# Optimization experiments

Measured on AMD Instinct MI355X. Metric: run time of the kernel, lower is better.

## Reference

```python
import jax, jax.numpy as jnp
import numpy as np

N = 50000      # num nodes
E0 = 400000    # raw directed edges
F = 64         # latent_dim (in and per-head out)
H = 2          # num_heads
L = 2          # num_layers
NEG_SLOPE = 0.2


def _build_edges(src_raw, dst_raw):
    # dgl.to_bidirected(dgl.graph((src,dst))) then add_self_loop
    s = np.asarray(src_raw, dtype=np.int64)
    d = np.asarray(dst_raw, dtype=np.int64)
    s2 = np.concatenate([s, d])
    d2 = np.concatenate([d, s])
    code = np.unique(s2 * N + d2)                      # dedupe (bidirected simple graph)
    s2, d2 = code // N, code % N
    keep = s2 != d2                                    # drop existing self loops
    s2, d2 = s2[keep], d2[keep]
    loops = np.arange(N, dtype=np.int64)
    s2 = np.concatenate([s2, loops])
    d2 = np.concatenate([d2, loops])
    return jnp.asarray(s2, jnp.int32), jnp.asarray(d2, jnp.int32)


def setup_inputs() -> dict:
    key = jax.random.key(0)
    kh, ks, kd, kw1, kb1, kw2, kb2, ka = jax.random.split(key, 8)
    src_raw = jax.random.randint(ks, (E0,), 0, N, dtype=jnp.int32)
    dst_raw = jax.random.randint(kd, (E0,), 0, N, dtype=jnp.int32)
    src, dst = _build_edges(np.asarray(src_raw), np.asarray(dst_raw))
    h = jax.random.normal(kh, (N, F), dtype=jnp.float32)
    scale = 1.0 / np.sqrt(F)
    Wsrc = jax.random.normal(kw1, (L, F, H * F), dtype=jnp.float32) * scale
    bsrc = jnp.zeros((L, H * F), dtype=jnp.float32)
    Wdst = jax.random.normal(kw2, (L, F, H * F), dtype=jnp.float32) * scale
    bdst = jnp.zeros((L, H * F), dtype=jnp.float32)
    attn = jax.random.normal(ka, (L, H, F), dtype=jnp.float32) * scale
    return {"h": h, "Wsrc": Wsrc, "bsrc": bsrc, "Wdst": Wdst, "bdst": bdst,
            "attn": attn, "src": src, "dst": dst}


def _gatv2_layer(h, Wsrc, bsrc, Wdst, bdst, attn, src, dst):
    # h: [N,F] -> per-head projections [N,H,F]
    fs = (h @ Wsrc + bsrc).reshape(N, H, F)
    fd = (h @ Wdst + bdst).reshape(N, H, F)
    # per-edge GATv2 logits: a^T leaky_relu(W_s h_u + W_d h_v)
    e = jax.nn.leaky_relu(fs[src] + fd[dst], NEG_SLOPE)      # [E,H,F]
    logits = jnp.einsum("ehf,hf->eh", e, attn)               # [E,H]
    # edge-softmax over incoming edges of each dst node
    m = jax.ops.segment_max(logits, dst, num_segments=N)     # [N,H]
    ex = jnp.exp(logits - m[dst])
    denom = jax.ops.segment_sum(ex, dst, num_segments=N)     # [N,H]
    alpha = ex / denom[dst]                                  # [E,H]
    # scatter-weighted aggregation
    out = jax.ops.segment_sum(alpha[:, :, None] * fs[src], dst, num_segments=N)  # [N,H,F]
    return out.mean(axis=1)                                  # head mean -> [N,F]


def reference(h, Wsrc, bsrc, Wdst, bdst, attn, src, dst):
    for l in range(L):
        h = _gatv2_layer(h, Wsrc[l], bsrc[l], Wdst[l], bdst[l], attn[l], src, dst)
    return h
```

## Files before the change

### kernel.cpp

```cpp
#include <hip/hip_runtime.h>


#define RLN2 1.4426950408889634f

typedef _Float16 half8v __attribute__((ext_vector_type(8)));
typedef _Float16 half2v __attribute__((ext_vector_type(2)));

template <int CTRL>
__device__ __forceinline__ float dpp_add(float x) {
  return x + __int_as_float(__builtin_amdgcn_update_dpp(
                 0, __float_as_int(x), CTRL, 0xF, 0xF, true));
}

__device__ __forceinline__ float xor16_add(float x) {
  return x + __int_as_float(
                 __builtin_amdgcn_ds_swizzle(__float_as_int(x), 0x401F));
}

__device__ __forceinline__ float dot2(half2v a, half2v b, float c) {
#if __has_builtin(__builtin_amdgcn_fdot2)
  return __builtin_amdgcn_fdot2(a, b, c, false);
#else
  return fmaf((float)a.x, (float)b.x, fmaf((float)a.y, (float)b.y, c));
#endif
}

__global__ void rowstart_kernel(const int* __restrict__ src,
                                int* __restrict__ row_start, int EM, int n) {
  int v = blockIdx.x * blockDim.x + threadIdx.x;
  if (v > n) return;
  if (v == n) { row_start[n] = EM; return; }
  int lo = 0, hi = EM;
  while (lo < hi) {
    int mid = (lo + hi) >> 1;
    if (src[mid] < v) lo = mid + 1; else hi = mid;
  }
  row_start[v] = lo;
}

__global__ __launch_bounds__(512) void proj2_kernel(
    const float* __restrict__ hin, const float* __restrict__ Ws,
    const float* __restrict__ bs, const float* __restrict__ Wd,
    const float* __restrict__ bd, _Float16* __restrict__ fs16,
    _Float16* __restrict__ fd16, int n) {
  __shared__ float lds[12544];
  int tid = threadIdx.x;
  int tile = blockIdx.x >> 1;
  int half = blockIdx.x & 1;
  int fb = half * 32;
  int row0 = tile * 64;

  const float4* Ws4 = (const float4*)Ws;
  const float4* Wd4 = (const float4*)Wd;
#pragma unroll
  for (int t = 0; t < 2; ++t) {
    int g = tid + t * 512;
    int k = g >> 4, part = (g >> 3) & 1, c4 = g & 7;
    int srcf4 = k * 32 + part * 16 + half * 8 + c4;
    float4 vs = Ws4[srcf4];
    float4 vd = Wd4[srcf4];
    int base = k * 64 + 8 * c4 + part;
    lds[base + 0] = vs.x; lds[base + 2] = vs.y;
    lds[base + 4] = vs.z; lds[base + 6] = vs.w;
    lds[4096 + base + 0] = vd.x; lds[4096 + base + 2] = vd.y;
    lds[4096 + base + 4] = vd.z; lds[4096 + base + 6] = vd.w;
  }
  const float4* h4 = (const float4*)hin;
#pragma unroll
  for (int t = 0; t < 2; ++t) {
    int idx = tid + t * 512;
    int r = idx >> 4, c = idx & 15;
    int rr = min(row0 + r, n - 1);
    *(float4*)&lds[8192 + r * 68 + c * 4] = h4[(size_t)rr * 16 + c];
  }
  __syncthreads();

  const float* WsL = lds;
  const float* WdL = lds + 4096;
  const float* hL = lds + 8192;

  int jh = tid & 15;
  int rg = tid >> 4;
  int r0 = rg * 2;

  float4 as0 = make_float4(0, 0, 0, 0), as1 = make_float4(0, 0, 0, 0);
  float4 ad0 = make_float4(0, 0, 0, 0), ad1 = make_float4(0, 0, 0, 0);

#pragma unroll 4
  for (int k4 = 0; k4 < 16; ++k4) {
    float4 hv0 = *(const float4*)&hL[r0 * 68 + k4 * 4];
    float4 hv1 = *(const float4*)&hL[(r0 + 1) * 68 + k4 * 4];
    float h0a[4] = {hv0.x, hv0.y, hv0.z, hv0.w};
    float h1a[4] = {hv1.x, hv1.y, hv1.z, hv1.w};
#pragma unroll
    for (int kk = 0; kk < 4; ++kk) {
      int k = k4 * 4 + kk;
      float4 ws = *(const float4*)&WsL[k * 64 + jh * 4];
      float4 wd = *(const float4*)&WdL[k * 64 + jh * 4];
      as0.x = fmaf(h0a[kk], ws.x, as0.x); as0.y = fmaf(h0a[kk], ws.y, as0.y);
      as0.z = fmaf(h0a[kk], ws.z, as0.z); as0.w = fmaf(h0a[kk], ws.w, as0.w);
      as1.x = fmaf(h1a[kk], ws.x, as1.x); as1.y = fmaf(h1a[kk], ws.y, as1.y);
      as1.z = fmaf(h1a[kk], ws.z, as1.z); as1.w = fmaf(h1a[kk], ws.w, as1.w);
      ad0.x = fmaf(h0a[kk], wd.x, ad0.x); ad0.y = fmaf(h0a[kk], wd.y, ad0.y);
      ad0.z = fmaf(h0a[kk], wd.z, ad0.z); ad0.w = fmaf(h0a[kk], wd.w, ad0.w);
      ad1.x = fmaf(h1a[kk], wd.x, ad1.x); ad1.y = fmaf(h1a[kk], wd.y, ad1.y);
      ad1.z = fmaf(h1a[kk], wd.z, ad1.z); ad1.w = fmaf(h1a[kk], wd.w, ad1.w);
    }
  }

  int j0 = fb + 2 * jh, j1 = j0 + 1;
  float4 bsv = make_float4(bs[j0], bs[64 + j0], bs[j1], bs[64 + j1]);
  float4 bdv = make_float4(bd[j0], bd[64 + j0], bd[j1], bd[64 + j1]);
  int c0 = j0 >> 2, o = j0 & 3;
  int base = c0 * 8 + o;
#pragma unroll
  for (int r = 0; r < 2; ++r) {
    int rr = row0 + r0 + r;
    if (rr < n) {
      float4 a = r ? as1 : as0;
      float4 d = r ? ad1 : ad0;
      half2v s_h0 = {(_Float16)(a.x + bsv.x), (_Float16)(a.z + bsv.z)};
      half2v s_h1 = {(_Float16)(a.y + bsv.y), (_Float16)(a.w + bsv.w)};
      half2v d_h0 = {(_Float16)(d.x + bdv.x), (_Float16)(d.z + bdv.z)};
      half2v d_h1 = {(_Float16)(d.y + bdv.y), (_Float16)(d.w + bdv.w)};
      *(half2v*)&fs16[(size_t)rr * 128 + base] = s_h0;
      *(half2v*)&fs16[(size_t)rr * 128 + base + 4] = s_h1;
      *(half2v*)&fd16[(size_t)rr * 128 + base] = d_h0;
      *(half2v*)&fd16[(size_t)rr * 128 + base + 4] = d_h1;
    }
  }
}

__global__ __launch_bounds__(256) void gat_node_kernel(
    const _Float16* __restrict__ fs16, const _Float16* __restrict__ fd16,
    const float* __restrict__ attn, const int* __restrict__ row_start,
    const int* __restrict__ nbr, float* __restrict__ out, int n) {
  int wid = (int)((blockIdx.x * 256 + threadIdx.x) >> 6);
  int lane = threadIdx.x & 63;
  if (wid >= n) return;
  int lp = lane & 15;
  int slot = lane >> 4;

  half2v a0lo = {(_Float16)(attn[4 * lp] * RLN2),
                 (_Float16)(attn[4 * lp + 1] * RLN2)};
  half2v a0hi = {(_Float16)(attn[4 * lp + 2] * RLN2),
                 (_Float16)(attn[4 * lp + 3] * RLN2)};
  half2v a1lo = {(_Float16)(attn[64 + 4 * lp] * RLN2),
                 (_Float16)(attn[64 + 4 * lp + 1] * RLN2)};
  half2v a1hi = {(_Float16)(attn[64 + 4 * lp + 2] * RLN2),
                 (_Float16)(attn[64 + 4 * lp + 3] * RLN2)};
  const half8v c02 = {(_Float16)0.2f, (_Float16)0.2f, (_Float16)0.2f,
                      (_Float16)0.2f, (_Float16)0.2f, (_Float16)0.2f,
                      (_Float16)0.2f, (_Float16)0.2f};

  const half8v* fsC = (const half8v*)fs16;
  const half8v* fdC = (const half8v*)fd16;
  half8v fdh = fdC[(size_t)wid * 16 + lp];

  float4 acc0 = make_float4(0, 0, 0, 0), acc1 = make_float4(0, 0, 0, 0);
  float d0 = 0.f, d1 = 0.f;

#define EDGE_COMPUTE(xv, kill_cond)                                        \
  {                                                                        \
    half8v t = (xv) + fdh;                                                 \
    half8v m = __builtin_elementwise_max(t, t * c02);                      \
    float p0 = dot2(__builtin_shufflevector(m, m, 0, 1), a0lo, 0.f);       \
    p0 = dot2(__builtin_shufflevector(m, m, 2, 3), a0hi, p0);              \
    float p1 = dot2(__builtin_shufflevector(m, m, 4, 5), a1lo, 0.f);       \
    p1 = dot2(__builtin_shufflevector(m, m, 6, 7), a1hi, p1);              \
    p0 = dpp_add<0xB1>(p0);  p1 = dpp_add<0xB1>(p1);                       \
    p0 = dpp_add<0x4E>(p0);  p1 = dpp_add<0x4E>(p1);                       \
    p0 = dpp_add<0x141>(p0); p1 = dpp_add<0x141>(p1);                      \
    p0 = dpp_add<0x140>(p0); p1 = dpp_add<0x140>(p1);                      \
    float w0 = __builtin_amdgcn_exp2f(p0);                                 \
    float w1 = __builtin_amdgcn_exp2f(p1);                                 \
    if (kill_cond) { w0 = 0.f; w1 = 0.f; }                                 \
    d0 += w0; d1 += w1;                                                    \
    acc0.x = fmaf(w0, (float)(xv)[0], acc0.x);                             \
    acc0.y = fmaf(w0, (float)(xv)[1], acc0.y);                             \
    acc0.z = fmaf(w0, (float)(xv)[2], acc0.z);                             \
    acc0.w = fmaf(w0, (float)(xv)[3], acc0.w);                             \
    acc1.x = fmaf(w1, (float)(xv)[4], acc1.x);                             \
    acc1.y = fmaf(w1, (float)(xv)[5], acc1.y);                             \
    acc1.z = fmaf(w1, (float)(xv)[6], acc1.z);                             \
    acc1.w = fmaf(w1, (float)(xv)[7], acc1.w);                             \
  }

  {
    half8v xs = fsC[(size_t)wid * 16 + lp];
    EDGE_COMPUTE(xs, (slot != 0));
  }

  int e0 = row_start[wid], e1 = row_start[wid + 1];
  if (e0 < e1) {
    int last = e1 - 1;
    int u0 = nbr[min(e0 + slot, last)];
    int u1 = nbr[min(e0 + 4 + slot, last)];
    int u2 = nbr[min(e0 + 8 + slot, last)];
    half8v x0 = fsC[(size_t)u0 * 16 + lp];
    half8v x1 = fsC[(size_t)u1 * 16 + lp];
    half8v x2 = fsC[(size_t)u2 * 16 + lp];

    int i = e0;
    for (; i + 8 <= e1; i += 8) {
      int ua = nbr[min(i + 12 + slot, last)];
      int ub = nbr[min(i + 16 + slot, last)];
      half8v xa = fsC[(size_t)ua * 16 + lp];
      EDGE_COMPUTE(x0, (i + slot >= e1));
      half8v xb = fsC[(size_t)ub * 16 + lp];
      EDGE_COMPUTE(x1, (i + 4 + slot >= e1));
      x0 = x2; x1 = xa; x2 = xb;
    }
    if (i < e1) {
      EDGE_COMPUTE(x0, (i + slot >= e1));
      i += 4;
      if (i < e1) EDGE_COMPUTE(x1, (i + slot >= e1));
    }
  }

  acc0.x = xor16_add(acc0.x); acc0.y = xor16_add(acc0.y);
  acc0.z = xor16_add(acc0.z); acc0.w = xor16_add(acc0.w);
  acc1.x = xor16_add(acc1.x); acc1.y = xor16_add(acc1.y);
  acc1.z = xor16_add(acc1.z); acc1.w = xor16_add(acc1.w);
  d0 = xor16_add(d0); d1 = xor16_add(d1);
  acc0.x += __shfl_xor(acc0.x, 32, 64); acc0.y += __shfl_xor(acc0.y, 32, 64);
  acc0.z += __shfl_xor(acc0.z, 32, 64); acc0.w += __shfl_xor(acc0.w, 32, 64);
  acc1.x += __shfl_xor(acc1.x, 32, 64); acc1.y += __shfl_xor(acc1.y, 32, 64);
  acc1.z += __shfl_xor(acc1.z, 32, 64); acc1.w += __shfl_xor(acc1.w, 32, 64);
  d0 += __shfl_xor(d0, 32, 64); d1 += __shfl_xor(d1, 32, 64);

  if (lane < 16) {
    float rd0 = 1.0f / d0, rd1 = 1.0f / d1;
    float4 o;
    o.x = 0.5f * (acc0.x * rd0 + acc1.x * rd1);
    o.y = 0.5f * (acc0.y * rd0 + acc1.y * rd1);
    o.z = 0.5f * (acc0.z * rd0 + acc1.z * rd1);
    o.w = 0.5f * (acc0.w * rd0 + acc1.w * rd1);
    ((float4*)out)[(size_t)wid * 16 + lp] = o;
  }
#undef EDGE_COMPUTE
}

extern "C" void kernel_launch(void* const* d_in, const int* in_sizes, int n_in,
                              void* d_out, int out_size, void* d_ws, size_t ws_size,
                              hipStream_t stream) {
  const float* h    = (const float*)d_in[0];
  const float* Wsrc = (const float*)d_in[1];
  const float* bsrc = (const float*)d_in[2];
  const float* Wdst = (const float*)d_in[3];
  const float* bdst = (const float*)d_in[4];
  const float* attn = (const float*)d_in[5];
  const int*   src  = (const int*)d_in[6];
  const int*   dst  = (const int*)d_in[7];
  int E = in_sizes[6];
  int N = in_sizes[0] / 64;
  int EM = E - N;
  float* out = (float*)d_out;

  _Float16* fs16      = (_Float16*)d_ws;
  _Float16* fd16      = fs16 + (size_t)N * 128;
  int*      row_start = (int*)(fd16 + (size_t)N * 128);

  rowstart_kernel<<<(N + 256) / 256, 256, 0, stream>>>(src, row_start, EM, N);

  int pb = ((N + 63) / 64) * 2;
  int nb = (N + 3) / 4;
  for (int l = 0; l < 2; ++l) {
    const float* hin = (l == 0) ? h : out;
    proj2_kernel<<<pb, 512, 0, stream>>>(hin, Wsrc + (size_t)l * 64 * 128,
                                         bsrc + (size_t)l * 128,
                                         Wdst + (size_t)l * 64 * 128,
                                         bdst + (size_t)l * 128, fs16, fd16, N);
    gat_node_kernel<<<nb, 256, 0, stream>>>(fs16, fd16, attn + (size_t)l * 128,
                                            row_start, dst, out, N);
  }
}
```

Before: 156.4 us.

## Make GAT node kernel grid-stride persistent with next-node prefetch

The node aggregation kernel now launches a fixed grid of 2048 blocks, and each wave walks nodes with a grid stride instead of using one wave per node. While processing the current node, it loads the next node's row bounds and destination features ahead of time, hiding that latency. This also spreads the per-wave setup cost (attention weight conversion) over many nodes. The trade-off is fewer waves in flight, possible load imbalance across waves, and extra registers for the prefetched state.

```diff
diff --git a/kernel.cpp b/kernel.cpp
--- a/kernel.cpp
+++ b/kernel.cpp
@@ -134,12 +134,12 @@
 __global__ __launch_bounds__(256) void gat_node_kernel(
     const _Float16* __restrict__ fs16, const _Float16* __restrict__ fd16,
     const float* __restrict__ attn, const int* __restrict__ row_start,
-    const int* __restrict__ nbr, float* __restrict__ out, int n) {
-  int wid = (int)((blockIdx.x * 256 + threadIdx.x) >> 6);
+    const int* __restrict__ nbr, float* __restrict__ out, int n, int nw) {
+  int gwid = (int)((blockIdx.x * 256 + threadIdx.x) >> 6);
   int lane = threadIdx.x & 63;
-  if (wid >= n) return;
   int lp = lane & 15;
   int slot = lane >> 4;
+  if (gwid >= n) return;
 
   half2v a0lo = {(_Float16)(attn[4 * lp] * RLN2),
                  (_Float16)(attn[4 * lp + 1] * RLN2)};
@@ -155,10 +155,6 @@
 
   const half8v* fsC = (const half8v*)fs16;
   const half8v* fdC = (const half8v*)fd16;
-  half8v fdh = fdC[(size_t)wid * 16 + lp];
-
-  float4 acc0 = make_float4(0, 0, 0, 0), acc1 = make_float4(0, 0, 0, 0);
-  float d0 = 0.f, d1 = 0.f;
 
 #define EDGE_COMPUTE(xv, kill_cond)                                        \
   {                                                                        \
@@ -186,57 +182,77 @@
     acc1.w = fmaf(w1, (float)(xv)[7], acc1.w);                             \
   }
 
-  {
-    half8v xs = fsC[(size_t)wid * 16 + lp];
-    EDGE_COMPUTE(xs, (slot != 0));
-  }
-
-  int e0 = row_start[wid], e1 = row_start[wid + 1];
-  if (e0 < e1) {
-    int last = e1 - 1;
-    int u0 = nbr[min(e0 + slot, last)];
-    int u1 = nbr[min(e0 + 4 + slot, last)];
-    int u2 = nbr[min(e0 + 8 + slot, last)];
-    half8v x0 = fsC[(size_t)u0 * 16 + lp];
-    half8v x1 = fsC[(size_t)u1 * 16 + lp];
-    half8v x2 = fsC[(size_t)u2 * 16 + lp];
-
-    int i = e0;
-    for (; i + 8 <= e1; i += 8) {
-      int ua = nbr[min(i + 12 + slot, last)];
-      int ub = nbr[min(i + 16 + slot, last)];
-      half8v xa = fsC[(size_t)ua * 16 + lp];
-      EDGE_COMPUTE(x0, (i + slot >= e1));
-      half8v xb = fsC[(size_t)ub * 16 + lp];
-      EDGE_COMPUTE(x1, (i + 4 + slot >= e1));
-      x0 = x2; x1 = xa; x2 = xb;
-    }
-    if (i < e1) {
-      EDGE_COMPUTE(x0, (i + slot >= e1));
-      i += 4;
-      if (i < e1) EDGE_COMPUTE(x1, (i + slot >= e1));
-    }
-  }
-
-  acc0.x = xor16_add(acc0.x); acc0.y = xor16_add(acc0.y);
-  acc0.z = xor16_add(acc0.z); acc0.w = xor16_add(acc0.w);
-  acc1.x = xor16_add(acc1.x); acc1.y = xor16_add(acc1.y);
-  acc1.z = xor16_add(acc1.z); acc1.w = xor16_add(acc1.w);
-  d0 = xor16_add(d0); d1 = xor16_add(d1);
-  acc0.x += __shfl_xor(acc0.x, 32, 64); acc0.y += __shfl_xor(acc0.y, 32, 64);
-  acc0.z += __shfl_xor(acc0.z, 32, 64); acc0.w += __shfl_xor(acc0.w, 32, 64);
-  acc1.x += __shfl_xor(acc1.x, 32, 64); acc1.y += __shfl_xor(acc1.y, 32, 64);
-  acc1.z += __shfl_xor(acc1.z, 32, 64); acc1.w += __shfl_xor(acc1.w, 32, 64);
-  d0 += __shfl_xor(d0, 32, 64); d1 += __shfl_xor(d1, 32, 64);
-
-  if (lane < 16) {
-    float rd0 = 1.0f / d0, rd1 = 1.0f / d1;
-    float4 o;
-    o.x = 0.5f * (acc0.x * rd0 + acc1.x * rd1);
-    o.y = 0.5f * (acc0.y * rd0 + acc1.y * rd1);
-    o.z = 0.5f * (acc0.z * rd0 + acc1.z * rd1);
-    o.w = 0.5f * (acc0.w * rd0 + acc1.w * rd1);
-    ((float4*)out)[(size_t)wid * 16 + lp] = o;
+  int v = gwid;
+  int e0 = row_start[v], e1 = row_start[v + 1];
+  half8v fdh = fdC[(size_t)v * 16 + lp];
+
+  while (true) {
+    int vn = v + nw;
+    int e0n = 0, e1n = 0;
+    half8v fdhn = fdh;
+    if (vn < n) {
+      e0n = row_start[vn];
+      e1n = row_start[vn + 1];
+      fdhn = fdC[(size_t)vn * 16 + lp];
+    }
+
+    float4 acc0 = make_float4(0, 0, 0, 0), acc1 = make_float4(0, 0, 0, 0);
+    float d0 = 0.f, d1 = 0.f;
+
+    {
+      half8v xs = fsC[(size_t)v * 16 + lp];
+      EDGE_COMPUTE(xs, (slot != 0));
+    }
+
+    if (e0 < e1) {
+      int last = e1 - 1;
+      int u0 = nbr[min(e0 + slot, last)];
+      int u1 = nbr[min(e0 + 4 + slot, last)];
+      int u2 = nbr[min(e0 + 8 + slot, last)];
+      half8v x0 = fsC[(size_t)u0 * 16 + lp];
+      half8v x1 = fsC[(size_t)u1 * 16 + lp];
+      half8v x2 = fsC[(size_t)u2 * 16 + lp];
+
+      int i = e0;
+      for (; i + 8 <= e1; i += 8) {
+        int ua = nbr[min(i + 12 + slot, last)];
+        int ub = nbr[min(i + 16 + slot, last)];
+        half8v xa = fsC[(size_t)ua * 16 + lp];
+        EDGE_COMPUTE(x0, (i + slot >= e1));
+        half8v xb = fsC[(size_t)ub * 16 + lp];
+        EDGE_COMPUTE(x1, (i + 4 + slot >= e1));
+        x0 = x2; x1 = xa; x2 = xb;
+      }
+      if (i < e1) {
+        EDGE_COMPUTE(x0, (i + slot >= e1));
+        i += 4;
+        if (i < e1) EDGE_COMPUTE(x1, (i + slot >= e1));
+      }
+    }
+
+    acc0.x = xor16_add(acc0.x); acc0.y = xor16_add(acc0.y);
+    acc0.z = xor16_add(acc0.z); acc0.w = xor16_add(acc0.w);
+    acc1.x = xor16_add(acc1.x); acc1.y = xor16_add(acc1.y);
+    acc1.z = xor16_add(acc1.z); acc1.w = xor16_add(acc1.w);
+    d0 = xor16_add(d0); d1 = xor16_add(d1);
+    acc0.x += __shfl_xor(acc0.x, 32, 64); acc0.y += __shfl_xor(acc0.y, 32, 64);
+    acc0.z += __shfl_xor(acc0.z, 32, 64); acc0.w += __shfl_xor(acc0.w, 32, 64);
+    acc1.x += __shfl_xor(acc1.x, 32, 64); acc1.y += __shfl_xor(acc1.y, 32, 64);
+    acc1.z += __shfl_xor(acc1.z, 32, 64); acc1.w += __shfl_xor(acc1.w, 32, 64);
+    d0 += __shfl_xor(d0, 32, 64); d1 += __shfl_xor(d1, 32, 64);
+
+    if (lane < 16) {
+      float rd0 = 1.0f / d0, rd1 = 1.0f / d1;
+      float4 o;
+      o.x = 0.5f * (acc0.x * rd0 + acc1.x * rd1);
+      o.y = 0.5f * (acc0.y * rd0 + acc1.y * rd1);
+      o.z = 0.5f * (acc0.z * rd0 + acc1.z * rd1);
+      o.w = 0.5f * (acc0.w * rd0 + acc1.w * rd1);
+      ((float4*)out)[(size_t)v * 16 + lp] = o;
+    }
+
+    if (vn >= n) break;
+    v = vn; e0 = e0n; e1 = e1n; fdh = fdhn;
   }
 #undef EDGE_COMPUTE
 }
@@ -264,14 +280,15 @@
   rowstart_kernel<<<(N + 256) / 256, 256, 0, stream>>>(src, row_start, EM, N);
 
   int pb = ((N + 63) / 64) * 2;
-  int nb = (N + 3) / 4;
+  int gb = 2048;
+  int nw = gb * 4;
   for (int l = 0; l < 2; ++l) {
     const float* hin = (l == 0) ? h : out;
     proj2_kernel<<<pb, 512, 0, stream>>>(hin, Wsrc + (size_t)l * 64 * 128,
                                          bsrc + (size_t)l * 128,
                                          Wdst + (size_t)l * 64 * 128,
                                          bdst + (size_t)l * 128, fs16, fd16, N);
-    gat_node_kernel<<<nb, 256, 0, stream>>>(fs16, fd16, attn + (size_t)l * 128,
-                                            row_start, dst, out, N);
-  }
-}
+    gat_node_kernel<<<gb, 256, 0, stream>>>(fs16, fd16, attn + (size_t)l * 128,
+                                            row_start, dst, out, N, nw);
+  }
+}
```

Result: slower. 172.0 us (+9.9%).
